# Kernel optimization log

Measured on AMD Instinct MI355X. Metric: run time of the kernel, lower is better.

Reference implementation:

```python
import jax, jax.numpy as jnp
import numpy as np

N_NODES = 307
U = 100          # gru units / GAT out dim
D_IN = 3         # per-node input features
F_IN = U + D_IN  # 103, GATv2 input dim
NEG_SLOPE = 0.2


def setup_inputs() -> dict:
    key = jax.random.key(0)
    ks = jax.random.split(key, 12)
    B, E = 256, 4096
    inputs = jax.random.normal(ks[0], (B, N_NODES * D_IN), dtype=jnp.float32)
    state = jax.random.normal(ks[1], (B, N_NODES * U), dtype=jnp.float32)
    src = jax.random.randint(ks[2], (E,), 0, N_NODES, dtype=jnp.int32)
    dst = jax.random.randint(ks[3], (E,), 0, N_NODES, dtype=jnp.int32)
    def glorot(k, shape):
        lim = float(np.sqrt(6.0 / (shape[0] + shape[1])))
        return jax.random.uniform(k, shape, jnp.float32, -lim, lim)
    return {
        "inputs": inputs, "state": state, "src": src, "dst": dst,
        "Wl": glorot(ks[4], (F_IN, U)),        # GATv2 lin_l (source)
        "Wr": glorot(ks[5], (F_IN, U)),        # GATv2 lin_r (target)
        "att": jax.random.normal(ks[6], (U,), jnp.float32) * 0.1,
        "gat_bias": jnp.zeros((U,), jnp.float32),
        "bias_gc": jnp.zeros((U,), jnp.float32),   # self.bias_1 added in _gc3
        "W_gru1": glorot(ks[7], (F_IN, 2 * U)),    # GRULinear(100,200)
        "b_gru1": jnp.zeros((2 * U,), jnp.float32),
        "W_gru2": glorot(ks[8], (F_IN, U)),        # GRULinear(100,100)
        "b_gru2": jnp.zeros((U,), jnp.float32),
    }


def _gru_linear(inputs, hidden, W, b):
    # cat((inputs[B,N,3], hidden[B,N,U]), -1) @ W + b
    B = hidden.shape[0]
    x = jnp.concatenate([inputs.reshape(B, N_NODES, D_IN),
                         hidden.reshape(B, N_NODES, U)], axis=2)
    return jnp.einsum('bnf,fo->bno', x, W) + b


def _gatv2(x, src, dst, Wl, Wr, att, gat_bias):
    # x: (B, N, F_IN); PyG GATv2Conv with heads=1, add_self_loops=True
    loops = jnp.arange(N_NODES, dtype=src.dtype)
    s = jnp.concatenate([src, loops])
    d = jnp.concatenate([dst, loops])
    xl = jnp.einsum('bnf,fu->bnu', x, Wl)  # source transform
    xr = jnp.einsum('bnf,fu->bnu', x, Wr)  # target transform

    def per_sample(xl_b, xr_b):
        m = xl_b[s]                                        # (E', U)
        e = jax.nn.leaky_relu(m + xr_b[d], NEG_SLOPE) @ att  # (E',)
        emax = jax.ops.segment_max(e, d, num_segments=N_NODES)
        ex = jnp.exp(e - emax[d])
        denom = jax.ops.segment_sum(ex, d, num_segments=N_NODES)
        alpha = ex / denom[d]
        return jax.ops.segment_sum(alpha[:, None] * m, d, num_segments=N_NODES)

    out = jax.vmap(per_sample)(xl, xr)  # (B, N, U)
    return out + gat_bias


def reference(inputs, state, src, dst, Wl, Wr, att, gat_bias, bias_gc,
              W_gru1, b_gru1, W_gru2, b_gru2):
    B = state.shape[0]
    # _gc3: cat([state, inputs]) -> GATv2 per sample -> + bias_1
    x = jnp.concatenate([state.reshape(B, N_NODES, U),
                         inputs.reshape(B, N_NODES, D_IN)], axis=2)
    st = _gatv2(x, src, dst, Wl, Wr, att, gat_bias) + bias_gc
    st = st.reshape(B, N_NODES * U)
    # GRU gating
    value = jax.nn.sigmoid(_gru_linear(inputs, st, W_gru1, b_gru1))  # (B,N,2U)
    r, u = jnp.split(value, 2, axis=-1)
    r = r.reshape(B, N_NODES * U)
    u = u.reshape(B, N_NODES * U)
    c = jnp.tanh(_gru_linear(inputs, r * st, W_gru2, b_gru2)).reshape(B, N_NODES * U)
    return u * st + (1.0 - u) * c
```

## Files before the change

kernel.cpp:

```cpp
#include <hip/hip_runtime.h>
#include <math.h>

#define NN 307
#define UU 100
#define DD 3
#define UP 104
#define UNIT_W 14336
#define SC_CAP 4608
#define EI_CAP 4416
#define NTILE 20
#define NT 512

typedef _Float16 f16;
typedef f16  f16x2 __attribute__((ext_vector_type(2)));
typedef f16  f16x4 __attribute__((ext_vector_type(4)));
typedef f16  f16x8 __attribute__((ext_vector_type(8)));
typedef float f32x4 __attribute__((ext_vector_type(4)));
typedef unsigned short u16;

__global__ __launch_bounds__(256)
void pack_w_k(const float* __restrict__ Wl, const float* __restrict__ Wr,
              const float* __restrict__ Wg1, const float* __restrict__ Wg2,
              f16* __restrict__ Wp)
{
    const int idx = blockIdx.x * 256 + threadIdx.x;
    const int u   = idx / UNIT_W;
    const int rem = idx - u * UNIT_W;
    const int e   = rem & 7;
    const int l   = (rem >> 3) & 63;
    const int sj  = rem >> 9;
    const int s   = sj / 7, j = sj - 7 * s;
    const int col = j * 16 + (l & 15);
    const int k   = (s * 4 + (l >> 4)) * 8 + e;
    float v = 0.f;
    if (col < UU && k < UU + DD) {
        if (u == 0)      v = Wl[k * UU + col];
        else if (u == 1) v = Wr[k * UU + col];
        else {
            const int kk = (k < UU) ? (k + DD) : (k - UU);
            if (u == 2)      v = Wg1[kk * (2 * UU) + col];
            else if (u == 3) v = Wg1[kk * (2 * UU) + UU + col];
            else             v = Wg2[kk * UU + col];
        }
    }
    Wp[idx] = (f16)v;
}

__global__ __launch_bounds__(64)
void csr_count_k(const int* __restrict__ dst, int E, int* offs)
{
    const int d = blockIdx.x;
    const int lane = threadIdx.x;
    const int Etot = E + NN;
    int c = 0;
    for (int base = 0; base < Etot; base += 64) {
        const int e = base + lane;
        if (e < Etot) {
            const int de = (e < E) ? dst[e] : (e - E);
            c += (de == d) ? 1 : 0;
        }
    }
    #pragma unroll
    for (int m = 1; m < 64; m <<= 1) c += __shfl_xor(c, m, 64);
    if (lane == 0) {
        offs[d + 1] = c;
        if (d == 0) offs[0] = 0;
    }
}

__global__ __launch_bounds__(512)
void csr_scan_k(int* offs)
{
    __shared__ int c[512];
    const int t = threadIdx.x;
    c[t] = (t < NN) ? offs[t + 1] : 0;
    __syncthreads();
    #pragma unroll
    for (int off = 1; off < 512; off <<= 1) {
        const int v = (t >= off) ? c[t - off] : 0;
        __syncthreads();
        c[t] += v;
        __syncthreads();
    }
    if (t < NN) offs[t + 1] = c[t];
    if (t == 0) offs[0] = 0;
}

__global__ __launch_bounds__(64)
void csr_fill_k(const int* __restrict__ src, const int* __restrict__ dst,
                int E, const int* __restrict__ offs,
                int* eidx, int* ddst)
{
    const int d = blockIdx.x;
    const int lane = threadIdx.x;
    const int Etot = E + NN;
    int w = offs[d];
    for (int base = 0; base < Etot; base += 64) {
        const int e = base + lane;
        bool match = false;
        int se = 0;
        if (e < Etot) {
            const int de = (e < E) ? dst[e] : (e - E);
            se           = (e < E) ? src[e] : (e - E);
            match = (de == d);
        }
        const unsigned long long mask = __ballot(match);
        if (match) {
            const int pos = w + __popcll(mask & ((1ULL << lane) - 1ULL));
            eidx[pos] = se;
            ddst[pos] = d;
        }
        w += __popcll(mask);
    }
}

__device__ __forceinline__ void mma_unit1(const f16x8 (&af)[4],
                                          const f16* __restrict__ Wu,
                                          int l, f32x4 (&acc)[7])
{
    #pragma unroll
    for (int s = 0; s < 4; ++s) {
        #pragma unroll
        for (int j = 0; j < 7; ++j) {
            const f16x8 bv = *(const f16x8*)(Wu + (((s * 7 + j) * 64 + l) << 3));
            acc[j] = __builtin_amdgcn_mfma_f32_16x16x32_f16(af[s], bv, acc[j], 0, 0, 0);
        }
        __builtin_amdgcn_sched_barrier(0);
    }
}

__device__ __forceinline__ void mma_unit_nb(const f16x8 (&af)[4],
                                            const f16* __restrict__ Wu,
                                            int l, f32x4 (&acc)[7])
{
    #pragma unroll
    for (int s = 0; s < 4; ++s)
        #pragma unroll
        for (int j = 0; j < 7; ++j) {
            const f16x8 bv = *(const f16x8*)(Wu + (((s * 7 + j) * 64 + l) << 3));
            acc[j] = __builtin_amdgcn_mfma_f32_16x16x32_f16(af[s], bv, acc[j], 0, 0, 0);
        }
}

__device__ __forceinline__ void z7(f32x4 (&acc)[7])
{
    #pragma unroll
    for (int j = 0; j < 7; ++j) acc[j] = (f32x4)0.f;
}

__device__ __forceinline__ float fast_sigmoid(float x)
{
    return __fdividef(1.f, 1.f + __expf(-x));
}

__device__ __forceinline__ float fast_tanh(float x)
{
    return 1.f - __fdividef(2.f, __expf(2.f * x) + 1.f);
}

__global__ __launch_bounds__(NT)
__attribute__((amdgpu_waves_per_eu(2)))
void gat_all_k(const float* __restrict__ state, const float* __restrict__ inputs,
               const f16* __restrict__ Wp, const float* __restrict__ att,
               const float* __restrict__ gb, const float* __restrict__ bgc,
               const int* __restrict__ offs, const int* __restrict__ eidx,
               const int* __restrict__ ddst, int Etot,
               f16* __restrict__ stg)
{
    __shared__ f16   xl_s[NN * UP];
    __shared__ f16   xr_s[NN * UP];
    __shared__ float sc_s[SC_CAP];
    __shared__ u16   ei_s[EI_CAP];
    __shared__ f16   att_s[UP];

    const int b   = blockIdx.x;
    const int tid = threadIdx.x;
    const int w = tid >> 6, l = tid & 63, lr = l & 15, lk = l >> 4;
    const float* stf = state  + (size_t)b * NN * UU;
    const float* inb = inputs + (size_t)b * NN * DD;
    f16* stb = stg + (size_t)b * NN * UP;

    for (int q = tid; q < Etot; q += NT) ei_s[q] = (u16)eidx[q];
    for (int q = tid; q < 2 * NN; q += NT) {
        const int rr = (q < NN) ? q : (q - NN);
        f16* p = (q < NN) ? xl_s : xr_s;
        *(f16x4*)&p[rr * UP + 100] = (f16x4)(f16)0.f;
    }
    if (tid < UP) att_s[tid] = (tid < UU) ? (f16)att[tid] : (f16)0.f;

    for (int tile = w; tile < NTILE; tile += 8) {
        const int row  = tile * 16 + lr;
        const int crow = (row < NN) ? row : (NN - 1);
        const float* bf = stf + (size_t)crow * UU;
        f16x8 af[4];
        #pragma unroll
        for (int s = 0; s < 3; ++s) {
            const int kb = s * 4 + lk;
            const float4 x0 = *(const float4*)(bf + kb * 8);
            const float4 x1 = *(const float4*)(bf + kb * 8 + 4);
            f16x8 v;
            v[0]=(f16)x0.x; v[1]=(f16)x0.y; v[2]=(f16)x0.z; v[3]=(f16)x0.w;
            v[4]=(f16)x1.x; v[5]=(f16)x1.y; v[6]=(f16)x1.z; v[7]=(f16)x1.w;
            af[s] = v;
        }
        {
            f16x8 v = (f16x8)(f16)0.f;
            if (lk == 0) {
                const float4 x0 = *(const float4*)(bf + 96);
                v[0]=(f16)x0.x; v[1]=(f16)x0.y; v[2]=(f16)x0.z; v[3]=(f16)x0.w;
                v[4] = (f16)inb[(size_t)crow * DD + 0];
                v[5] = (f16)inb[(size_t)crow * DD + 1];
                v[6] = (f16)inb[(size_t)crow * DD + 2];
                v[7] = (f16)0.f;
            }
            af[3] = v;
        }
        __builtin_amdgcn_sched_barrier(0);
        #pragma unroll
        for (int u = 0; u < 2; ++u) {
            f32x4 acc[7];
            z7(acc);
            mma_unit1(af, Wp + (size_t)u * UNIT_W, l, acc);
            f16* dst = u ? xr_s : xl_s;
            #pragma unroll
            for (int j = 0; j < 7; ++j) {
                const int col = j * 16 + lr;
                if (col >= UU) continue;
                #pragma unroll
                for (int r = 0; r < 4; ++r) {
                    const int grow = tile * 16 + lk * 4 + r;
                    if (grow < NN) dst[grow * UP + col] = (f16)acc[j][r];
                }
            }
        }
    }
    __syncthreads();

    for (int i = tid; i < Etot; i += NT) {
        const int s = ei_s[i];
        const int d = ddst[i];
        const f16x8* a8 = (const f16x8*)&xl_s[s * UP];
        const f16x8* r8 = (const f16x8*)&xr_s[d * UP];
        float p0 = 0.f, p1 = 0.f;
        #pragma unroll 4
        for (int c = 0; c < 13; ++c) {
            const f16x8 x  = a8[c] + r8[c];
            const f16x8 xm = x * (f16)0.2f;
            const f16x8 y  = __builtin_elementwise_max(x, xm);
            const f16x2* y2  = (const f16x2*)&y;
            const f16x2* at2 = (const f16x2*)&att_s[c * 8];
#if __has_builtin(__builtin_amdgcn_fdot2)
            p0 = __builtin_amdgcn_fdot2(y2[0], at2[0], p0, false);
            p1 = __builtin_amdgcn_fdot2(y2[1], at2[1], p1, false);
            p0 = __builtin_amdgcn_fdot2(y2[2], at2[2], p0, false);
            p1 = __builtin_amdgcn_fdot2(y2[3], at2[3], p1, false);
#else
            #pragma unroll
            for (int q = 0; q < 4; ++q) {
                p0 += (float)y2[q][0] * (float)at2[q][0];
                p1 += (float)y2[q][1] * (float)at2[q][1];
            }
#endif
        }
        sc_s[i] = p0 + p1;
    }
    __syncthreads();

    if (tid < NN) {
        const int e0 = offs[tid], e1 = offs[tid + 1];
        float mx = -1e30f;
        for (int e = e0; e < e1; ++e) mx = fmaxf(mx, sc_s[e]);
        float dn = 0.f;
        for (int e = e0; e < e1; ++e) {
            const float ex = __expf(sc_s[e] - mx);
            sc_s[e] = ex;
            dn += ex;
        }
        const float inv = 1.f / dn;
        for (int e = e0; e < e1; ++e) sc_s[e] *= inv;
    }
    __syncthreads();

    {
        const int g   = tid >> 4;
        const int sub = tid & 15;
        const bool fa = (sub < 13);
        float bias_r[8];
        #pragma unroll
        for (int k = 0; k < 8; ++k) {
            const int f = sub * 8 + k;
            bias_r[k] = (fa && f < UU) ? (gb[f] + bgc[f]) : 0.f;
        }
        for (int d = g; d < NN; d += 32) {
            const int e0 = offs[d], e1 = offs[d + 1];
            float acc[8] = {0.f, 0.f, 0.f, 0.f, 0.f, 0.f, 0.f, 0.f};
            for (int e = e0; e < e1; ++e) {
                const float alpha = sc_s[e];
                const int s = ei_s[e];
                if (fa) {
                    const f16x8 m = *(const f16x8*)&xl_s[s * UP + sub * 8];
                    #pragma unroll
                    for (int k = 0; k < 8; ++k) acc[k] += alpha * (float)m[k];
                }
            }
            if (fa) {
                f16x8 o;
                #pragma unroll
                for (int k = 0; k < 8; ++k) o[k] = (f16)(acc[k] + bias_r[k]);
                *(f16x8*)(stb + (size_t)d * UP + sub * 8) = o;
            }
        }
    }
}

__global__ __launch_bounds__(256, 4)
void gru3_k(const f16* __restrict__ st, const float* __restrict__ inp,
            const f16* __restrict__ Wp2 ,
            const float* __restrict__ bg1, const float* __restrict__ bg2,
            float* __restrict__ out, int M)
{
    __shared__ f16 st_s[64 * UP];
    __shared__ f16 rst_s[64 * UP];

    const int tid = threadIdx.x;
    const int w = tid >> 6, l = tid & 63, lr = l & 15, lk = l >> 4;
    const int rb = blockIdx.x * 64 + w * 16;
    const int lbase = w * 16;

    #pragma unroll
    for (int p = 0; p < 4; ++p) {
        const int idx = p * 64 + l;
        const int row = idx >> 4, ch = idx & 15;
        if (ch < 13) {
            int gr = rb + row; if (gr >= M) gr = M - 1;
            *(f16x8*)&st_s[(lbase + row) * UP + ch * 8] =
                *(const f16x8*)(st + (size_t)gr * UP + ch * 8);
        }
    }

    int crow = rb + lr; if (crow >= M) crow = M - 1;
    const f16* bh = &st_s[(lbase + lr) * UP];
    f16x8 af[4];
    #pragma unroll
    for (int s = 0; s < 3; ++s)
        af[s] = *(const f16x8*)(bh + (s * 4 + lk) * 8);
    {
        f16x8 v = (f16x8)(f16)0.f;
        if (lk == 0) {
            v = *(const f16x8*)(bh + 96);
            v[4] = (f16)inp[(size_t)crow * DD + 0];
            v[5] = (f16)inp[(size_t)crow * DD + 1];
            v[6] = (f16)inp[(size_t)crow * DD + 2];
            v[7] = (f16)0.f;
        }
        af[3] = v;
    }

    f32x4 acc[7];

    z7(acc);
    mma_unit_nb(af, Wp2, l, acc);
    #pragma unroll
    for (int j = 0; j < 7; ++j) {
        const int col = j * 16 + lr;
        if (col >= UU) continue;
        const float bR = bg1[col];
        #pragma unroll
        for (int r = 0; r < 4; ++r) {
            const int grow = rb + lk * 4 + r;
            const int lrow = lbase + lk * 4 + r;
            if (grow < M) {
                const float stv = (float)st_s[lrow * UP + col];
                const float sg = fast_sigmoid(acc[j][r] + bR);
                rst_s[lrow * UP + col] = (f16)(sg * stv);
            }
        }
    }
    if (l < 16) {
        const int grow2 = rb + l;
        const int lrow2 = lbase + l;
        if (grow2 < M) {
            rst_s[lrow2 * UP + 100] = (f16)inp[(size_t)grow2 * DD + 0];
            rst_s[lrow2 * UP + 101] = (f16)inp[(size_t)grow2 * DD + 1];
            rst_s[lrow2 * UP + 102] = (f16)inp[(size_t)grow2 * DD + 2];
            rst_s[lrow2 * UP + 103] = (f16)0.f;
        }
    }

    z7(acc);
    mma_unit_nb(af, Wp2 + UNIT_W, l, acc);
    f16x4 uh[7];
    #pragma unroll
    for (int j = 0; j < 7; ++j) {
        const int col = j * 16 + lr;
        const float bU = (col < UU) ? bg1[UU + col] : 0.f;
        #pragma unroll
        for (int r = 0; r < 4; ++r)
            uh[j][r] = (f16)fast_sigmoid(acc[j][r] + bU);
    }

    f16x8 af2[4];
    #pragma unroll
    for (int s = 0; s < 3; ++s)
        af2[s] = *(const f16x8*)&rst_s[(lbase + lr) * UP + (s * 4 + lk) * 8];
    af2[3] = (lk == 0) ? *(const f16x8*)&rst_s[(lbase + lr) * UP + 96]
                       : (f16x8)(f16)0.f;

    z7(acc);
    mma_unit_nb(af2, Wp2 + 2 * UNIT_W, l, acc);
    #pragma unroll
    for (int j = 0; j < 7; ++j) {
        const int col = j * 16 + lr;
        if (col >= UU) continue;
        const float bC = bg2[col];
        #pragma unroll
        for (int r = 0; r < 4; ++r) {
            const int grow = rb + lk * 4 + r;
            const int lrow = lbase + lk * 4 + r;
            if (grow < M) {
                const float c = fast_tanh(acc[j][r] + bC);
                const float u = (float)uh[j][r];
                const float stv = (float)st_s[lrow * UP + col];
                out[(size_t)grow * UU + col] = u * stv + (1.f - u) * c;
            }
        }
    }
}

extern "C" void kernel_launch(void* const* d_in, const int* in_sizes, int n_in,
                              void* d_out, int out_size, void* d_ws, size_t ws_size,
                              hipStream_t stream)
{
    const float* inputs   = (const float*)d_in[0];
    const float* state    = (const float*)d_in[1];
    const int*   src      = (const int*)  d_in[2];
    const int*   dst      = (const int*)  d_in[3];
    const float* Wl       = (const float*)d_in[4];
    const float* Wr       = (const float*)d_in[5];
    const float* att      = (const float*)d_in[6];
    const float* gat_bias = (const float*)d_in[7];
    const float* bias_gc  = (const float*)d_in[8];
    const float* Wg1      = (const float*)d_in[9];
    const float* bg1      = (const float*)d_in[10];
    const float* Wg2      = (const float*)d_in[11];
    const float* bg2      = (const float*)d_in[12];

    const int E = in_sizes[2];
    const int B = in_sizes[1] / (NN * UU);
    const int M = B * NN;
    const int Etot = E + NN;

    char* ws = (char*)d_ws;
    f16* Wp   = (f16*)ws;
    int* offs = (int*)(ws + 5 * UNIT_W * sizeof(f16));
    int* eidx = offs + (NN + 1);
    int* ddst = eidx + (Etot + 64);
    f16* st_h = (f16*)(ws + (256 << 10));
    float* out = (float*)d_out;

    pack_w_k<<<280, 256, 0, stream>>>(Wl, Wr, Wg1, Wg2, Wp);
    csr_count_k<<<NN, 64, 0, stream>>>(dst, E, offs);
    csr_scan_k<<<1, 512, 0, stream>>>(offs);
    csr_fill_k<<<NN, 64, 0, stream>>>(src, dst, E, offs, eidx, ddst);

    gat_all_k<<<B, NT, 0, stream>>>(state, inputs, Wp, att,
        gat_bias, bias_gc, offs, eidx, ddst, Etot, st_h);

    gru3_k<<<(M + 63) / 64, 256, 0, stream>>>(st_h, inputs,
        Wp + 2 * (size_t)UNIT_W, bg1, bg2, out, M);
}
```

Measured before the change: 159.0 us.

## Split GAT into a standalone xl/xr GEMM and a destination-halved attention kernel

```diff
diff --git a/kernel.cpp b/kernel.cpp
--- a/kernel.cpp
+++ b/kernel.cpp
@@ -6,10 +6,9 @@
 #define DD 3
 #define UP 104
 #define UNIT_W 14336
-#define SC_CAP 4608
-#define EI_CAP 4416
-#define NTILE 20
+#define HCAP 2560
 #define NT 512
+#define NGRP (NT / 16)
 
 typedef _Float16 f16;
 typedef f16  f16x2 __attribute__((ext_vector_type(2)));
@@ -114,21 +113,6 @@
     }
 }
 
-__device__ __forceinline__ void mma_unit1(const f16x8 (&af)[4],
-                                          const f16* __restrict__ Wu,
-                                          int l, f32x4 (&acc)[7])
-{
-    #pragma unroll
-    for (int s = 0; s < 4; ++s) {
-        #pragma unroll
-        for (int j = 0; j < 7; ++j) {
-            const f16x8 bv = *(const f16x8*)(Wu + (((s * 7 + j) * 64 + l) << 3));
-            acc[j] = __builtin_amdgcn_mfma_f32_16x16x32_f16(af[s], bv, acc[j], 0, 0, 0);
-        }
-        __builtin_amdgcn_sched_barrier(0);
-    }
-}
-
 __device__ __forceinline__ void mma_unit_nb(const f16x8 (&af)[4],
                                             const f16* __restrict__ Wu,
                                             int l, f32x4 (&acc)[7])
@@ -158,158 +142,185 @@
     return 1.f - __fdividef(2.f, __expf(2.f * x) + 1.f);
 }
 
-__global__ __launch_bounds__(NT)
-__attribute__((amdgpu_waves_per_eu(2)))
-void gat_all_k(const float* __restrict__ state, const float* __restrict__ inputs,
-               const f16* __restrict__ Wp, const float* __restrict__ att,
-               const float* __restrict__ gb, const float* __restrict__ bgc,
-               const int* __restrict__ offs, const int* __restrict__ eidx,
-               const int* __restrict__ ddst, int Etot,
-               f16* __restrict__ stg)
-{
-    __shared__ f16   xl_s[NN * UP];
-    __shared__ f16   xr_s[NN * UP];
-    __shared__ float sc_s[SC_CAP];
-    __shared__ u16   ei_s[EI_CAP];
-    __shared__ f16   att_s[UP];
-
-    const int b   = blockIdx.x;
+__global__ __launch_bounds__(256, 4)
+void gemm_xlxr_k(const float* __restrict__ state, const float* __restrict__ inp,
+                 const f16* __restrict__ Wp,
+                 f16* __restrict__ xl, f16* __restrict__ xr, int M)
+{
     const int tid = threadIdx.x;
     const int w = tid >> 6, l = tid & 63, lr = l & 15, lk = l >> 4;
-    const float* stf = state  + (size_t)b * NN * UU;
-    const float* inb = inputs + (size_t)b * NN * DD;
+    const int rb = blockIdx.x * 64 + w * 16;
+    int crow = rb + lr; if (crow >= M) crow = M - 1;
+    const float* bf = state + (size_t)crow * UU;
+
+    f16x8 af[4];
+    #pragma unroll
+    for (int s = 0; s < 3; ++s) {
+        const int kb = s * 4 + lk;
+        const float4 x0 = *(const float4*)(bf + kb * 8);
+        const float4 x1 = *(const float4*)(bf + kb * 8 + 4);
+        f16x8 v;
+        v[0]=(f16)x0.x; v[1]=(f16)x0.y; v[2]=(f16)x0.z; v[3]=(f16)x0.w;
+        v[4]=(f16)x1.x; v[5]=(f16)x1.y; v[6]=(f16)x1.z; v[7]=(f16)x1.w;
+        af[s] = v;
+    }
+    {
+        f16x8 v = (f16x8)(f16)0.f;
+        if (lk == 0) {
+            const float4 x0 = *(const float4*)(bf + 96);
+            v[0]=(f16)x0.x; v[1]=(f16)x0.y; v[2]=(f16)x0.z; v[3]=(f16)x0.w;
+            v[4] = (f16)inp[(size_t)crow * DD + 0];
+            v[5] = (f16)inp[(size_t)crow * DD + 1];
+            v[6] = (f16)inp[(size_t)crow * DD + 2];
+            v[7] = (f16)0.f;
+        }
+        af[3] = v;
+    }
+
+    #pragma unroll
+    for (int u = 0; u < 2; ++u) {
+        f32x4 acc[7];
+        z7(acc);
+        mma_unit_nb(af, Wp + (size_t)u * UNIT_W, l, acc);
+        f16* dst = u ? xr : xl;
+        #pragma unroll
+        for (int j = 0; j < 7; ++j) {
+            const int col = j * 16 + lr;
+            if (col >= UU) continue;
+            #pragma unroll
+            for (int r = 0; r < 4; ++r) {
+                const int row = rb + lk * 4 + r;
+                if (row < M) dst[(size_t)row * UP + col] = (f16)acc[j][r];
+            }
+        }
+    }
+}
+
+__global__ __launch_bounds__(NT)
+__attribute__((amdgpu_waves_per_eu(4, 4)))
+void gat2h_k(const f16* __restrict__ xl, const f16* __restrict__ xr,
+             const int* __restrict__ offs, const int* __restrict__ eidx,
+             const int* __restrict__ ddst,
+             const float* __restrict__ att, const float* __restrict__ gb,
+             const float* __restrict__ bgc,
+             f16* __restrict__ stg)
+{
+    __shared__ f16   xl_s[NN * UP];
+    __shared__ float sc_s[HCAP];
+    __shared__ u16   ei_s[HCAP];
+    __shared__ f16   att_s[UP];
+
+    const int b   = blockIdx.x;
+    const int h   = blockIdx.y;
+    const int tid = threadIdx.x;
+    const int d0 = h * 154;
+    const int d1 = (h == 0) ? 154 : NN;
+    const f16* xlb = xl + (size_t)b * NN * UP;
+    const f16* xrb = xr + (size_t)b * NN * UP;
     f16* stb = stg + (size_t)b * NN * UP;
 
-    for (int q = tid; q < Etot; q += NT) ei_s[q] = (u16)eidx[q];
-    for (int q = tid; q < 2 * NN; q += NT) {
-        const int rr = (q < NN) ? q : (q - NN);
-        f16* p = (q < NN) ? xl_s : xr_s;
-        *(f16x4*)&p[rr * UP + 100] = (f16x4)(f16)0.f;
-    }
     if (tid < UP) att_s[tid] = (tid < UU) ? (f16)att[tid] : (f16)0.f;
-
-    for (int tile = w; tile < NTILE; tile += 8) {
-        const int row  = tile * 16 + lr;
-        const int crow = (row < NN) ? row : (NN - 1);
-        const float* bf = stf + (size_t)crow * UU;
-        f16x8 af[4];
-        #pragma unroll
-        for (int s = 0; s < 3; ++s) {
-            const int kb = s * 4 + lk;
-            const float4 x0 = *(const float4*)(bf + kb * 8);
-            const float4 x1 = *(const float4*)(bf + kb * 8 + 4);
-            f16x8 v;
-            v[0]=(f16)x0.x; v[1]=(f16)x0.y; v[2]=(f16)x0.z; v[3]=(f16)x0.w;
-            v[4]=(f16)x1.x; v[5]=(f16)x1.y; v[6]=(f16)x1.z; v[7]=(f16)x1.w;
-            af[s] = v;
-        }
+    for (int c = tid; c < NN * UP / 8; c += NT)
+        *(f16x8*)&xl_s[c * 8] = *(const f16x8*)&xlb[c * 8];
+
+    int dlo = d0;
+    while (dlo < d1) {
+        int dhi = d1;
+        const int base = offs[dlo];
+        if (offs[d1] - base > HCAP) {
+            int lo = dlo + 1, hi = d1;
+            while (lo < hi) {
+                const int mid = (lo + hi + 1) >> 1;
+                if (offs[mid] - base <= HCAP) lo = mid; else hi = mid - 1;
+            }
+            dhi = lo;
+        }
+        const int e0 = base, e1 = offs[dhi];
+        const int n  = e1 - e0;
+
+        for (int q = tid; q < n; q += NT) ei_s[q] = (u16)eidx[e0 + q];
+        __syncthreads();
+
+        for (int i = tid; i < n; i += NT) {
+            const int s = ei_s[i];
+            const int d = ddst[e0 + i];
+            const f16x8* a8 = (const f16x8*)&xl_s[s * UP];
+            const f16x8* r8 = (const f16x8*)(xrb + (size_t)d * UP);
+            float p0 = 0.f, p1 = 0.f;
+            #pragma unroll 4
+            for (int c = 0; c < 13; ++c) {
+                const f16x8 x  = a8[c] + r8[c];
+                const f16x8 xm = x * (f16)0.2f;
+                const f16x8 y  = __builtin_elementwise_max(x, xm);
+                const f16x2* y2  = (const f16x2*)&y;
+                const f16x2* at2 = (const f16x2*)&att_s[c * 8];
+#if __has_builtin(__builtin_amdgcn_fdot2)
+                p0 = __builtin_amdgcn_fdot2(y2[0], at2[0], p0, false);
+                p1 = __builtin_amdgcn_fdot2(y2[1], at2[1], p1, false);
+                p0 = __builtin_amdgcn_fdot2(y2[2], at2[2], p0, false);
+                p1 = __builtin_amdgcn_fdot2(y2[3], at2[3], p1, false);
+#else
+                #pragma unroll
+                for (int q = 0; q < 4; ++q) {
+                    p0 += (float)y2[q][0] * (float)at2[q][0];
+                    p1 += (float)y2[q][1] * (float)at2[q][1];
+                }
+#endif
+            }
+            sc_s[i] = p0 + p1;
+        }
+        __syncthreads();
+
         {
-            f16x8 v = (f16x8)(f16)0.f;
-            if (lk == 0) {
-                const float4 x0 = *(const float4*)(bf + 96);
-                v[0]=(f16)x0.x; v[1]=(f16)x0.y; v[2]=(f16)x0.z; v[3]=(f16)x0.w;
-                v[4] = (f16)inb[(size_t)crow * DD + 0];
-                v[5] = (f16)inb[(size_t)crow * DD + 1];
-                v[6] = (f16)inb[(size_t)crow * DD + 2];
-                v[7] = (f16)0.f;
-            }
-            af[3] = v;
-        }
-        __builtin_amdgcn_sched_barrier(0);
-        #pragma unroll
-        for (int u = 0; u < 2; ++u) {
-            f32x4 acc[7];
-            z7(acc);
-            mma_unit1(af, Wp + (size_t)u * UNIT_W, l, acc);
-            f16* dst = u ? xr_s : xl_s;
+            const int t = dlo + tid;
+            if (t < dhi) {
+                const int f0 = offs[t] - e0, f1 = offs[t + 1] - e0;
+                float mx = -1e30f;
+                for (int e = f0; e < f1; ++e) mx = fmaxf(mx, sc_s[e]);
+                float dn = 0.f;
+                for (int e = f0; e < f1; ++e) {
+                    const float ex = __expf(sc_s[e] - mx);
+                    sc_s[e] = ex;
+                    dn += ex;
+                }
+                const float inv = 1.f / dn;
+                for (int e = f0; e < f1; ++e) sc_s[e] *= inv;
+            }
+        }
+        __syncthreads();
+
+        {
+            const int g   = tid >> 4;
+            const int sub = tid & 15;
+            const bool fa = (sub < 13);
+            float bias_r[8];
             #pragma unroll
-            for (int j = 0; j < 7; ++j) {
-                const int col = j * 16 + lr;
-                if (col >= UU) continue;
-                #pragma unroll
-                for (int r = 0; r < 4; ++r) {
-                    const int grow = tile * 16 + lk * 4 + r;
-                    if (grow < NN) dst[grow * UP + col] = (f16)acc[j][r];
+            for (int k = 0; k < 8; ++k) {
+                const int f = sub * 8 + k;
+                bias_r[k] = (fa && f < UU) ? (gb[f] + bgc[f]) : 0.f;
+            }
+            for (int d = dlo + g; d < dhi; d += NGRP) {
+                const int f0 = offs[d] - e0, f1 = offs[d + 1] - e0;
+                float acc[8] = {0.f, 0.f, 0.f, 0.f, 0.f, 0.f, 0.f, 0.f};
+                for (int e = f0; e < f1; ++e) {
+                    const float alpha = sc_s[e];
+                    const int s = ei_s[e];
+                    if (fa) {
+                        const f16x8 m = *(const f16x8*)&xl_s[s * UP + sub * 8];
+                        #pragma unroll
+                        for (int k = 0; k < 8; ++k) acc[k] += alpha * (float)m[k];
+                    }
                 }
-            }
-        }
-    }
-    __syncthreads();
-
-    for (int i = tid; i < Etot; i += NT) {
-        const int s = ei_s[i];
-        const int d = ddst[i];
-        const f16x8* a8 = (const f16x8*)&xl_s[s * UP];
-        const f16x8* r8 = (const f16x8*)&xr_s[d * UP];
-        float p0 = 0.f, p1 = 0.f;
-        #pragma unroll 4
-        for (int c = 0; c < 13; ++c) {
-            const f16x8 x  = a8[c] + r8[c];
-            const f16x8 xm = x * (f16)0.2f;
-            const f16x8 y  = __builtin_elementwise_max(x, xm);
-            const f16x2* y2  = (const f16x2*)&y;
-            const f16x2* at2 = (const f16x2*)&att_s[c * 8];
-#if __has_builtin(__builtin_amdgcn_fdot2)
-            p0 = __builtin_amdgcn_fdot2(y2[0], at2[0], p0, false);
-            p1 = __builtin_amdgcn_fdot2(y2[1], at2[1], p1, false);
-            p0 = __builtin_amdgcn_fdot2(y2[2], at2[2], p0, false);
-            p1 = __builtin_amdgcn_fdot2(y2[3], at2[3], p1, false);
-#else
-            #pragma unroll
-            for (int q = 0; q < 4; ++q) {
-                p0 += (float)y2[q][0] * (float)at2[q][0];
-                p1 += (float)y2[q][1] * (float)at2[q][1];
-            }
-#endif
-        }
-        sc_s[i] = p0 + p1;
-    }
-    __syncthreads();
-
-    if (tid < NN) {
-        const int e0 = offs[tid], e1 = offs[tid + 1];
-        float mx = -1e30f;
-        for (int e = e0; e < e1; ++e) mx = fmaxf(mx, sc_s[e]);
-        float dn = 0.f;
-        for (int e = e0; e < e1; ++e) {
-            const float ex = __expf(sc_s[e] - mx);
-            sc_s[e] = ex;
-            dn += ex;
-        }
-        const float inv = 1.f / dn;
-        for (int e = e0; e < e1; ++e) sc_s[e] *= inv;
-    }
-    __syncthreads();
-
-    {
-        const int g   = tid >> 4;
-        const int sub = tid & 15;
-        const bool fa = (sub < 13);
-        float bias_r[8];
-        #pragma unroll
-        for (int k = 0; k < 8; ++k) {
-            const int f = sub * 8 + k;
-            bias_r[k] = (fa && f < UU) ? (gb[f] + bgc[f]) : 0.f;
-        }
-        for (int d = g; d < NN; d += 32) {
-            const int e0 = offs[d], e1 = offs[d + 1];
-            float acc[8] = {0.f, 0.f, 0.f, 0.f, 0.f, 0.f, 0.f, 0.f};
-            for (int e = e0; e < e1; ++e) {
-                const float alpha = sc_s[e];
-                const int s = ei_s[e];
                 if (fa) {
-                    const f16x8 m = *(const f16x8*)&xl_s[s * UP + sub * 8];
+                    f16x8 o;
                     #pragma unroll
-                    for (int k = 0; k < 8; ++k) acc[k] += alpha * (float)m[k];
+                    for (int k = 0; k < 8; ++k) o[k] = (f16)(acc[k] + bias_r[k]);
+                    *(f16x8*)(stb + (size_t)d * UP + sub * 8) = o;
                 }
             }
-            if (fa) {
-                f16x8 o;
-                #pragma unroll
-                for (int k = 0; k < 8; ++k) o[k] = (f16)(acc[k] + bias_r[k]);
-                *(f16x8*)(stb + (size_t)d * UP + sub * 8) = o;
-            }
-        }
+        }
+        dlo = dhi;
+        __syncthreads();
     }
 }
 
@@ -455,7 +466,9 @@
     int* offs = (int*)(ws + 5 * UNIT_W * sizeof(f16));
     int* eidx = offs + (NN + 1);
     int* ddst = eidx + (Etot + 64);
-    f16* st_h = (f16*)(ws + (256 << 10));
+    f16* xl_h = (f16*)(ws + (256 << 10));
+    f16* xr_h = xl_h + (size_t)M * UP;
+    f16* st_h = xr_h + (size_t)M * UP;
     float* out = (float*)d_out;
 
     pack_w_k<<<280, 256, 0, stream>>>(Wl, Wr, Wg1, Wg2, Wp);
@@ -463,8 +476,11 @@
     csr_scan_k<<<1, 512, 0, stream>>>(offs);
     csr_fill_k<<<NN, 64, 0, stream>>>(src, dst, E, offs, eidx, ddst);
 
-    gat_all_k<<<B, NT, 0, stream>>>(state, inputs, Wp, att,
-        gat_bias, bias_gc, offs, eidx, ddst, Etot, st_h);
+    gemm_xlxr_k<<<(M + 63) / 64, 256, 0, stream>>>(state, inputs, Wp,
+                                                   xl_h, xr_h, M);
+
+    gat2h_k<<<dim3(B, 2), NT, 0, stream>>>(xl_h, xr_h, offs, eidx, ddst,
+                                           att, gat_bias, bias_gc, st_h);
 
     gru3_k<<<(M + 63) / 64, 256, 0, stream>>>(st_h, inputs,
         Wp + 2 * (size_t)UNIT_W, bg1, bg2, out, M);
```

Result: no change. 156.0 us (-1.9%).
